# Optimization experiments

Measured on AMD Instinct MI355X. Metric: run time of the kernel, lower is better.

The kernel has to match this reference:

```python
import jax, jax.numpy as jnp
import numpy as np
import math

WS = 7  # window size
NUM_HEADS = 6

def _relative_position_index(ws):
    coords = np.stack(np.meshgrid(np.arange(ws), np.arange(ws), indexing='ij'))  # 2,ws,ws
    cf = coords.reshape(2, -1)
    rel = cf[:, :, None] - cf[:, None, :]            # 2,N,N
    rel = rel.transpose(1, 2, 0).astype(np.int64)    # N,N,2
    rel[:, :, 0] += ws - 1
    rel[:, :, 1] += ws - 1
    rel[:, :, 0] *= 2 * ws - 1
    return jnp.asarray(rel.sum(-1))                  # N,N

RPI = _relative_position_index(WS)

def setup_inputs() -> dict:
    key = jax.random.key(0)
    ks = jax.random.split(key, 6)
    C = 192
    return {
        'x': jax.random.normal(ks[0], (32, 3136, C), dtype=jnp.float32),
        'gamma': jnp.ones((C,), dtype=jnp.float32),
        'rpb_table': jax.random.normal(ks[1], (169, NUM_HEADS), dtype=jnp.float32) * 0.02,
        'qkv_w': jax.random.normal(ks[2], (3 * C, C), dtype=jnp.float32) * (1.0 / math.sqrt(C)),
        'qkv_b': jax.random.normal(ks[3], (3 * C,), dtype=jnp.float32) * 0.02,
        'proj_w': jax.random.normal(ks[4], (C, C), dtype=jnp.float32) * (1.0 / math.sqrt(C)),
        'proj_b': jax.random.normal(ks[5], (C,), dtype=jnp.float32) * 0.02,
    }

def reference(x, gamma, rpb_table, qkv_w, qkv_b, proj_w, proj_b):
    B_, N, C = x.shape
    H = W = int(math.isqrt(N))
    h = NUM_HEADS
    d = C // h
    scale = d ** -0.5
    ws = WS
    NW = ws * ws  # tokens per window (49)

    # LayerNorm (beta = 0)
    mu = jnp.mean(x, axis=-1, keepdims=True)
    var = jnp.var(x, axis=-1, keepdims=True)
    xn = (x - mu) * jax.lax.rsqrt(var + 1e-5) * gamma

    # window partition: (B_,H,W,C) -> (B_*nWh*nWw, ws*ws, C)
    xn = xn.reshape(B_, H // ws, ws, W // ws, ws, C)
    xw = xn.transpose(0, 1, 3, 2, 4, 5).reshape(-1, NW, C)
    BW = xw.shape[0]

    # qkv projection
    qkv = xw @ qkv_w.T + qkv_b                        # (BW, NW, 3C)
    qkv = qkv.reshape(BW, NW, 3, h, d).transpose(2, 0, 3, 1, 4)
    q, k, v = qkv[0], qkv[1], qkv[2]                  # (BW, h, NW, d)

    attn = jnp.einsum('bhnd,bhmd->bhnm', q * scale, k)
    bias = rpb_table[RPI.reshape(-1)].reshape(NW, NW, h).transpose(2, 0, 1)
    attn = jax.nn.softmax(attn + bias[None], axis=-1)

    out = jnp.einsum('bhnm,bhmd->bhnd', attn, v)      # (BW, h, NW, d)
    out = out.transpose(0, 2, 1, 3).reshape(BW, NW, C)
    out = out @ proj_w.T + proj_b

    # window reverse
    out = out.reshape(B_, H // ws, W // ws, ws, ws, C)
    out = out.transpose(0, 1, 3, 2, 4, 5).reshape(B_, H * W, C)
    return out
```

## Files before the change

### kernel.cpp

```cpp
#include <hip/hip_runtime.h>


typedef __bf16 bf16x8 __attribute__((ext_vector_type(8)));
typedef float  f32x4  __attribute__((ext_vector_type(4)));
union U128 { uint4 u; bf16x8 v; };

__device__ __forceinline__ f32x4 mfma16(bf16x8 a, bf16x8 b, f32x4 c){
  return __builtin_amdgcn_mfma_f32_16x16x32_bf16(a, b, c, 0, 0, 0);
}
__device__ __forceinline__ f32x4 f4zero(){
  f32x4 z; z[0]=0.f; z[1]=0.f; z[2]=0.f; z[3]=0.f; return z;
}
__device__ __forceinline__ unsigned short f2bf(float f){
  union{float f; unsigned int i;} x; x.f = f;
  unsigned int r = x.i + 0x7fffu + ((x.i >> 16) & 1u);
  return (unsigned short)(r >> 16);
}
__device__ __forceinline__ bf16x8 ldfrag(const unsigned short* p){
  U128 x; x.u = *(const uint4*)p; return x.v;
}
__device__ __forceinline__ int div7(int t){ return (t * 9363) >> 16; }

__global__ void wa_prep(const float* __restrict__ qkv_w, const float* __restrict__ proj_w,
                        const float* __restrict__ rpb,
                        unsigned short* __restrict__ wq, unsigned short* __restrict__ wp,
                        float* __restrict__ bt){
  int i = blockIdx.x * 256 + threadIdx.x;
  if (i < 576*192) wq[i] = f2bf(qkv_w[i]);
  if (i < 192*192) wp[i] = f2bf(proj_w[i]);
  if (i < 6*64*64){
    int head = i >> 12, t = (i >> 6) & 63, j = i & 63;
    int l16 = j >> 2, nt = j & 3;
    int col = nt*16 + l16;
    float v;
    if (t < 49 && col < 49){
      int tr = div7(t),   tc = t   - tr*7;
      int jr = div7(col), jc = col - jr*7;
      v = rpb[((tr - jr + 6)*13 + (tc - jc + 6))*6 + head];
    } else {
      v = (col >= 49) ? -3.0e38f : 0.0f;
    }
    bt[i] = v;
  }
}

__global__ __launch_bounds__(256, 8) void wa_ln(
    const float* __restrict__ x, const float* __restrict__ gamma,
    unsigned short* __restrict__ xng)
{
  const int tid  = threadIdx.x;
  const int wave = tid >> 6, lane = tid & 63;
  const int wid  = blockIdx.x * 4 + wave;
  const int wi   = wid >> 6, t = wid & 63;
  unsigned short* dst = xng + (size_t)wid * 192;
  if (t >= 49){
    if (lane < 24){ const uint4 z = {0u,0u,0u,0u}; *(uint4*)&dst[lane*8] = z; }
    return;
  }
  const int b = wi >> 6, wr = (wi >> 3) & 7, wc = wi & 7;
  const int tr = div7(t), tc = t - tr*7;
  const float* xt = x + ((size_t)b*3136 + (size_t)((wr*7 + tr)*56 + wc*7 + tc)) * 192;
  float v0 = xt[lane], v1 = xt[lane+64], v2 = xt[lane+128];
  float s  = v0 + v1 + v2;
  float sq = v0*v0 + v1*v1 + v2*v2;
#pragma unroll
  for (int off = 32; off > 0; off >>= 1){
    s  += __shfl_xor(s,  off);
    sq += __shfl_xor(sq, off);
  }
  float mu  = s * (1.0f/192.0f);
  float var = sq * (1.0f/192.0f) - mu*mu;
  float inv = rsqrtf(var + 1e-5f);
  dst[lane]      = f2bf((v0 - mu)*inv*gamma[lane]);
  dst[lane+64]   = f2bf((v1 - mu)*inv*gamma[lane+64]);
  dst[lane+128]  = f2bf((v2 - mu)*inv*gamma[lane+128]);
}

#define QKS 40
__global__ __launch_bounds__(384, 5) void wa_k1(
    const unsigned short* __restrict__ xng, const float* __restrict__ bt,
    const unsigned short* __restrict__ wq, const float* __restrict__ qkv_b,
    unsigned short* __restrict__ attn)
{
  __shared__ __align__(16) unsigned short qk[6*64*QKS];
  __shared__ __align__(16) unsigned short vt[3*32*72];

  const int blk  = blockIdx.x;
  const int wi   = blk >> 1;
  const int h0   = (blk & 1) * 3;
  const int b    = wi >> 6;
  const int wr   = (wi >> 3) & 7;
  const int wc   = wi & 7;
  const int tid  = threadIdx.x;
  const int wave = tid >> 6;
  const int lane = tid & 63;
  const int quad = lane >> 4;
  const int l16  = lane & 15;

  unsigned short* const qs = qk;
  unsigned short* const ks = qk + 3*64*QKS;

  {
    const int sec = wave >> 1;
    const int n0  = sec*192 + h0*32 + (wave & 1)*48;
    const unsigned short* xw = xng + (size_t)wi * 64 * 192;
    f32x4 acc[4][3];
#pragma unroll
    for (int mt = 0; mt < 4; mt++)
#pragma unroll
      for (int nt = 0; nt < 3; nt++) acc[mt][nt] = f4zero();

#pragma unroll
    for (int kt = 0; kt < 6; kt++){
      bf16x8 a[4], bw[3];
#pragma unroll
      for (int mt = 0; mt < 4; mt++)
        a[mt] = ldfrag(&xw[(size_t)(mt*16 + l16)*192 + kt*32 + quad*8]);
#pragma unroll
      for (int nt = 0; nt < 3; nt++)
        bw[nt] = ldfrag(&wq[(size_t)(n0 + nt*16 + l16)*192 + kt*32 + quad*8]);
#pragma unroll
      for (int mt = 0; mt < 4; mt++)
#pragma unroll
        for (int nt = 0; nt < 3; nt++)
          acc[mt][nt] = mfma16(a[mt], bw[nt], acc[mt][nt]);
    }
    const float scale = 0.17677669529663687f;
#pragma unroll
    for (int nt = 0; nt < 3; nt++){
      const int bc = (wave & 1)*48 + nt*16 + l16;
      const int hl2 = bc >> 5, d = bc & 31;
      const float bias = qkv_b[n0 + nt*16 + l16];
#pragma unroll
      for (int mt = 0; mt < 4; mt++)
#pragma unroll
        for (int r = 0; r < 4; r++){
          const int row = mt*16 + quad*4 + r;
          const float val = acc[mt][nt][r] + bias;
          if (sec == 0)      qs[(hl2*64 + row)*QKS + d] = f2bf(val * scale);
          else if (sec == 1) ks[(hl2*64 + row)*QKS + d] = f2bf(val);
          else               vt[(hl2*32 + d)*72 + row]  = f2bf(val);
        }
    }
  }
  __syncthreads();

  const int hl   = wave >> 1;
  const int half = wave & 1;
  const int head = h0 + hl;

  bf16x8 aq[2];
#pragma unroll
  for (int i = 0; i < 2; i++)
    aq[i] = ldfrag(&qs[(hl*64 + half*32 + i*16 + l16)*QKS + quad*8]);

  f32x4 s[2][4];
#pragma unroll
  for (int nt = 0; nt < 4; nt++){
    bf16x8 bk = ldfrag(&ks[(hl*64 + nt*16 + l16)*QKS + quad*8]);
#pragma unroll
    for (int i = 0; i < 2; i++)
      s[i][nt] = mfma16(aq[i], bk, f4zero());
  }

  f32x4 bias4[2][4];
#pragma unroll
  for (int i = 0; i < 2; i++)
#pragma unroll
    for (int r = 0; r < 4; r++){
      const int t = half*32 + i*16 + quad*4 + r;
      bias4[i][r] = *(const f32x4*)&bt[head*4096 + t*64 + l16*4];
    }

  __syncthreads();

  float linv[2][4];
#pragma unroll
  for (int i = 0; i < 2; i++)
#pragma unroll
    for (int r = 0; r < 4; r++){
      const f32x4 b4 = bias4[i][r];
#pragma unroll
      for (int nt = 0; nt < 4; nt++) s[i][nt][r] += b4[nt];
      float m = fmaxf(fmaxf(s[i][0][r], s[i][1][r]), fmaxf(s[i][2][r], s[i][3][r]));
#pragma unroll
      for (int off = 8; off > 0; off >>= 1) m = fmaxf(m, __shfl_xor(m, off));
      float l = 0.f;
      const int t = half*32 + i*16 + quad*4 + r;
#pragma unroll
      for (int nt = 0; nt < 4; nt++){
        float p = __expf(s[i][nt][r] - m);
        l += p;
        qk[hl*4608 + t*72 + nt*16 + l16] = f2bf(p);
      }
#pragma unroll
      for (int off = 8; off > 0; off >>= 1) l += __shfl_xor(l, off);
      linv[i][r] = 1.f / l;
    }

  f32x4 o[2][2];
#pragma unroll
  for (int i = 0; i < 2; i++)
#pragma unroll
    for (int n2 = 0; n2 < 2; n2++) o[i][n2] = f4zero();
#pragma unroll
  for (int kt = 0; kt < 2; kt++){
    bf16x8 ap[2], bv[2];
#pragma unroll
    for (int i = 0; i < 2; i++)
      ap[i] = ldfrag(&qk[hl*4608 + (half*32 + i*16 + l16)*72 + kt*32 + quad*8]);
#pragma unroll
    for (int n2 = 0; n2 < 2; n2++)
      bv[n2] = ldfrag(&vt[(hl*32 + n2*16 + l16)*72 + kt*32 + quad*8]);
#pragma unroll
    for (int i = 0; i < 2; i++)
#pragma unroll
      for (int n2 = 0; n2 < 2; n2++)
        o[i][n2] = mfma16(ap[i], bv[n2], o[i][n2]);
  }

#pragma unroll
  for (int i = 0; i < 2; i++)
#pragma unroll
    for (int r = 0; r < 4; r++){
      const int t = half*32 + i*16 + quad*4 + r;
      if (t < 49){
        const int tr = div7(t), tcc = t - tr*7;
        const size_t base =
          ((size_t)b*3136 + (size_t)((wr*7 + tr)*56 + wc*7 + tcc))*192 + head*32;
        const float inv = linv[i][r];
        attn[base + l16]      = f2bf(o[i][0][r] * inv);
        attn[base + 16 + l16] = f2bf(o[i][1][r] * inv);
      }
    }
}

__global__ __launch_bounds__(256, 4) void wa_k2(
    const unsigned short* __restrict__ a, const unsigned short* __restrict__ wp,
    const float* __restrict__ pb, float* __restrict__ out)
{
  const int mblk = blockIdx.x;
  const int nblk = blockIdx.y;
  const int tid  = threadIdx.x;
  const int wave = tid >> 6;
  const int lane = tid & 63;
  const int quad = lane >> 4;
  const int l16  = lane & 15;

  f32x4 acc[2][4];
#pragma unroll
  for (int i = 0; i < 2; i++)
#pragma unroll
    for (int nt = 0; nt < 4; nt++) acc[i][nt] = f4zero();

#pragma unroll
  for (int kt = 0; kt < 6; kt++){
    bf16x8 av[2], bw[4];
#pragma unroll
    for (int i = 0; i < 2; i++)
      av[i] = ldfrag(&a[(size_t)(mblk*128 + (wave*2 + i)*16 + l16)*192 + kt*32 + quad*8]);
#pragma unroll
    for (int nt = 0; nt < 4; nt++)
      bw[nt] = ldfrag(&wp[(size_t)(nblk*64 + nt*16 + l16)*192 + kt*32 + quad*8]);
#pragma unroll
    for (int i = 0; i < 2; i++)
#pragma unroll
      for (int nt = 0; nt < 4; nt++)
        acc[i][nt] = mfma16(av[i], bw[nt], acc[i][nt]);
  }

#pragma unroll
  for (int nt = 0; nt < 4; nt++){
    const int col = nblk*64 + nt*16 + l16;
    const float bias = pb[col];
#pragma unroll
    for (int i = 0; i < 2; i++)
#pragma unroll
      for (int r = 0; r < 4; r++){
        const int row = mblk*128 + (wave*2 + i)*16 + quad*4 + r;
        out[(size_t)row*192 + col] = acc[i][nt][r] + bias;
      }
  }
}

extern "C" void kernel_launch(void* const* d_in, const int* in_sizes, int n_in,
                              void* d_out, int out_size, void* d_ws, size_t ws_size,
                              hipStream_t stream) {
  (void)in_sizes; (void)n_in; (void)out_size; (void)ws_size;
  const float* x      = (const float*)d_in[0];
  const float* gamma  = (const float*)d_in[1];
  const float* rpb    = (const float*)d_in[2];
  const float* qkv_w  = (const float*)d_in[3];
  const float* qkv_b  = (const float*)d_in[4];
  const float* proj_w = (const float*)d_in[5];
  const float* proj_b = (const float*)d_in[6];

  unsigned short* wq   = (unsigned short*)d_ws;
  unsigned short* wp   = wq + 576*192;
  float* bt            = (float*)(wp + 192*192);
  unsigned short* attn = (unsigned short*)(bt + 6*64*64);

  unsigned short* xng = (unsigned short*)d_out;
  float* out = (float*)d_out;

  hipLaunchKernelGGL(wa_prep, dim3(432), dim3(256), 0, stream,
                     qkv_w, proj_w, rpb, wq, wp, bt);
  hipLaunchKernelGGL(wa_ln, dim3(32768), dim3(256), 0, stream,
                     x, gamma, xng);
  hipLaunchKernelGGL(wa_k1, dim3(4096), dim3(384), 0, stream,
                     xng, bt, wq, qkv_b, attn);
  hipLaunchKernelGGL(wa_k2, dim3(784, 3), dim3(256), 0, stream,
                     attn, wp, proj_b, out);
}
```

Baseline: 362.8 us.

## Merge prep into LayerNorm kernel and hoist all GEMM fragment loads

The weight-conversion and bias-table prep kernel is folded into the first 432 blocks of the LayerNorm kernel, which removes one launch. Both GEMM loops in wa_k1 and wa_k2 now load every A/B fragment up front, with a sched_barrier before the MFMA chain, so global-load latency overlaps instead of being serialised per k-step. wa_k1's occupancy hint drops from 5 to 4 to make room for the extra registers, and the bias-table loads are issued before the QK MFMAs. The trade-off is higher register pressure and lower occupancy.

```diff
diff --git a/kernel.cpp b/kernel.cpp
--- a/kernel.cpp
+++ b/kernel.cpp
@@ -21,34 +21,36 @@
 }
 __device__ __forceinline__ int div7(int t){ return (t * 9363) >> 16; }
 
-__global__ void wa_prep(const float* __restrict__ qkv_w, const float* __restrict__ proj_w,
-                        const float* __restrict__ rpb,
-                        unsigned short* __restrict__ wq, unsigned short* __restrict__ wp,
-                        float* __restrict__ bt){
-  int i = blockIdx.x * 256 + threadIdx.x;
-  if (i < 576*192) wq[i] = f2bf(qkv_w[i]);
-  if (i < 192*192) wp[i] = f2bf(proj_w[i]);
-  if (i < 6*64*64){
-    int head = i >> 12, t = (i >> 6) & 63, j = i & 63;
-    int l16 = j >> 2, nt = j & 3;
-    int col = nt*16 + l16;
-    float v;
-    if (t < 49 && col < 49){
-      int tr = div7(t),   tc = t   - tr*7;
-      int jr = div7(col), jc = col - jr*7;
-      v = rpb[((tr - jr + 6)*13 + (tc - jc + 6))*6 + head];
-    } else {
-      v = (col >= 49) ? -3.0e38f : 0.0f;
-    }
-    bt[i] = v;
-  }
-}
-
 __global__ __launch_bounds__(256, 8) void wa_ln(
     const float* __restrict__ x, const float* __restrict__ gamma,
-    unsigned short* __restrict__ xng)
+    unsigned short* __restrict__ xng,
+    const float* __restrict__ qkv_w, const float* __restrict__ proj_w,
+    const float* __restrict__ rpb,
+    unsigned short* __restrict__ wq, unsigned short* __restrict__ wp,
+    float* __restrict__ bt)
 {
   const int tid  = threadIdx.x;
+
+  if (blockIdx.x < 432){
+    int i = blockIdx.x * 256 + tid;
+    if (i < 576*192) wq[i] = f2bf(qkv_w[i]);
+    if (i < 192*192) wp[i] = f2bf(proj_w[i]);
+    if (i < 6*64*64){
+      int head = i >> 12, t = (i >> 6) & 63, j = i & 63;
+      int l16 = j >> 2, nt = j & 3;
+      int col = nt*16 + l16;
+      float v;
+      if (t < 49 && col < 49){
+        int tr = div7(t),   tc = t   - tr*7;
+        int jr = div7(col), jc = col - jr*7;
+        v = rpb[((tr - jr + 6)*13 + (tc - jc + 6))*6 + head];
+      } else {
+        v = (col >= 49) ? -3.0e38f : 0.0f;
+      }
+      bt[i] = v;
+    }
+  }
+
   const int wave = tid >> 6, lane = tid & 63;
   const int wid  = blockIdx.x * 4 + wave;
   const int wi   = wid >> 6, t = wid & 63;
@@ -77,7 +79,7 @@
 }
 
 #define QKS 40
-__global__ __launch_bounds__(384, 5) void wa_k1(
+__global__ __launch_bounds__(384, 4) void wa_k1(
     const unsigned short* __restrict__ xng, const float* __restrict__ bt,
     const unsigned short* __restrict__ wq, const float* __restrict__ qkv_b,
     unsigned short* __restrict__ attn)
@@ -104,6 +106,19 @@
     const int sec = wave >> 1;
     const int n0  = sec*192 + h0*32 + (wave & 1)*48;
     const unsigned short* xw = xng + (size_t)wi * 64 * 192;
+
+    bf16x8 a[6][4], bwf[6][3];
+#pragma unroll
+    for (int kt = 0; kt < 6; kt++){
+#pragma unroll
+      for (int mt = 0; mt < 4; mt++)
+        a[kt][mt] = ldfrag(&xw[(size_t)(mt*16 + l16)*192 + kt*32 + quad*8]);
+#pragma unroll
+      for (int nt = 0; nt < 3; nt++)
+        bwf[kt][nt] = ldfrag(&wq[(size_t)(n0 + nt*16 + l16)*192 + kt*32 + quad*8]);
+    }
+    __builtin_amdgcn_sched_barrier(0);
+
     f32x4 acc[4][3];
 #pragma unroll
     for (int mt = 0; mt < 4; mt++)
@@ -111,20 +126,13 @@
       for (int nt = 0; nt < 3; nt++) acc[mt][nt] = f4zero();
 
 #pragma unroll
-    for (int kt = 0; kt < 6; kt++){
-      bf16x8 a[4], bw[3];
+    for (int kt = 0; kt < 6; kt++)
 #pragma unroll
       for (int mt = 0; mt < 4; mt++)
-        a[mt] = ldfrag(&xw[(size_t)(mt*16 + l16)*192 + kt*32 + quad*8]);
-#pragma unroll
-      for (int nt = 0; nt < 3; nt++)
-        bw[nt] = ldfrag(&wq[(size_t)(n0 + nt*16 + l16)*192 + kt*32 + quad*8]);
-#pragma unroll
-      for (int mt = 0; mt < 4; mt++)
 #pragma unroll
         for (int nt = 0; nt < 3; nt++)
-          acc[mt][nt] = mfma16(a[mt], bw[nt], acc[mt][nt]);
-    }
+          acc[mt][nt] = mfma16(a[kt][mt], bwf[kt][nt], acc[mt][nt]);
+
     const float scale = 0.17677669529663687f;
 #pragma unroll
     for (int nt = 0; nt < 3; nt++){
@@ -149,20 +157,6 @@
   const int half = wave & 1;
   const int head = h0 + hl;
 
-  bf16x8 aq[2];
-#pragma unroll
-  for (int i = 0; i < 2; i++)
-    aq[i] = ldfrag(&qs[(hl*64 + half*32 + i*16 + l16)*QKS + quad*8]);
-
-  f32x4 s[2][4];
-#pragma unroll
-  for (int nt = 0; nt < 4; nt++){
-    bf16x8 bk = ldfrag(&ks[(hl*64 + nt*16 + l16)*QKS + quad*8]);
-#pragma unroll
-    for (int i = 0; i < 2; i++)
-      s[i][nt] = mfma16(aq[i], bk, f4zero());
-  }
-
   f32x4 bias4[2][4];
 #pragma unroll
   for (int i = 0; i < 2; i++)
@@ -171,6 +165,20 @@
       const int t = half*32 + i*16 + quad*4 + r;
       bias4[i][r] = *(const f32x4*)&bt[head*4096 + t*64 + l16*4];
     }
+
+  bf16x8 aq[2];
+#pragma unroll
+  for (int i = 0; i < 2; i++)
+    aq[i] = ldfrag(&qs[(hl*64 + half*32 + i*16 + l16)*QKS + quad*8]);
+
+  f32x4 s[2][4];
+#pragma unroll
+  for (int nt = 0; nt < 4; nt++){
+    bf16x8 bk = ldfrag(&ks[(hl*64 + nt*16 + l16)*QKS + quad*8]);
+#pragma unroll
+    for (int i = 0; i < 2; i++)
+      s[i][nt] = mfma16(aq[i], bk, f4zero());
+  }
 
   __syncthreads();
 
@@ -247,6 +255,18 @@
   const int quad = lane >> 4;
   const int l16  = lane & 15;
 
+  bf16x8 av[6][2], bw[6][4];
+#pragma unroll
+  for (int kt = 0; kt < 6; kt++){
+#pragma unroll
+    for (int i = 0; i < 2; i++)
+      av[kt][i] = ldfrag(&a[(size_t)(mblk*128 + (wave*2 + i)*16 + l16)*192 + kt*32 + quad*8]);
+#pragma unroll
+    for (int nt = 0; nt < 4; nt++)
+      bw[kt][nt] = ldfrag(&wp[(size_t)(nblk*64 + nt*16 + l16)*192 + kt*32 + quad*8]);
+  }
+  __builtin_amdgcn_sched_barrier(0);
+
   f32x4 acc[2][4];
 #pragma unroll
   for (int i = 0; i < 2; i++)
@@ -254,20 +274,12 @@
     for (int nt = 0; nt < 4; nt++) acc[i][nt] = f4zero();
 
 #pragma unroll
-  for (int kt = 0; kt < 6; kt++){
-    bf16x8 av[2], bw[4];
-#pragma unroll
-    for (int i = 0; i < 2; i++)
-      av[i] = ldfrag(&a[(size_t)(mblk*128 + (wave*2 + i)*16 + l16)*192 + kt*32 + quad*8]);
-#pragma unroll
-    for (int nt = 0; nt < 4; nt++)
-      bw[nt] = ldfrag(&wp[(size_t)(nblk*64 + nt*16 + l16)*192 + kt*32 + quad*8]);
+  for (int kt = 0; kt < 6; kt++)
 #pragma unroll
     for (int i = 0; i < 2; i++)
 #pragma unroll
       for (int nt = 0; nt < 4; nt++)
-        acc[i][nt] = mfma16(av[i], bw[nt], acc[i][nt]);
-  }
+        acc[i][nt] = mfma16(av[kt][i], bw[kt][nt], acc[i][nt]);
 
 #pragma unroll
   for (int nt = 0; nt < 4; nt++){
@@ -303,10 +315,8 @@
   unsigned short* xng = (unsigned short*)d_out;
   float* out = (float*)d_out;
 
-  hipLaunchKernelGGL(wa_prep, dim3(432), dim3(256), 0, stream,
-                     qkv_w, proj_w, rpb, wq, wp, bt);
   hipLaunchKernelGGL(wa_ln, dim3(32768), dim3(256), 0, stream,
-                     x, gamma, xng);
+                     x, gamma, xng, qkv_w, proj_w, rpb, wq, wp, bt);
   hipLaunchKernelGGL(wa_k1, dim3(4096), dim3(384), 0, stream,
                      xng, bt, wq, qkv_b, attn);
   hipLaunchKernelGGL(wa_k2, dim3(784, 3), dim3(256), 0, stream,
```

After: 481.4 us. 32.7% more time.
